# Optimization experiments

Hardware: AMD Instinct MI355X
Metric: run time of the kernel (lower is better)

The kernel has to match this reference:

```python
import jax, jax.numpy as jnp
import numpy as np

EPS = 1e-5  # F.instance_norm default eps


def _patch_attn(x, s):
    """Per-(b,c) instance norm over non-overlapping s x s patches, then sigmoid."""
    b, c, h, w = x.shape
    xr = x.reshape(b, c, h // s, s, w // s, s)
    m = jnp.mean(xr, axis=(3, 5), keepdims=True)
    v = jnp.mean((xr - m) ** 2, axis=(3, 5), keepdims=True)  # biased var, as in training-mode instance_norm
    a = jax.nn.sigmoid((xr - m) * jax.lax.rsqrt(v + EPS))
    return a.reshape(b, c, h, w)


def setup_inputs() -> dict:
    key = jax.random.key(0)
    x = jax.random.normal(key, (16, 64, 256, 256), dtype=jnp.float32)
    return {"x": x}


def reference(x):
    p = (2, 1, 0)
    b, c, h, w = x.shape
    out = x
    for pi in p:  # fixed 3 scales (structural loop, not data loop)
        s = h // (2 ** pi)
        attn = _patch_attn(out, s)
        out = 0.5 * out + 0.5 * (attn * out)
    return out
```

## Files before the change

kernel.cpp:

```cpp
#include <hip/hip_runtime.h>

#define PEPS  1e-5f
#define LOG2E 1.4426950408889634f

__device__ __forceinline__ float fast_rcp(float x) { return __builtin_amdgcn_rcpf(x); }

__device__ __forceinline__ float patch_one(float x, float nrs2, float mrs) {
    const float e = __builtin_amdgcn_exp2f(fmaf(x, nrs2, mrs));
    return x * fmaf(0.5f, fast_rcp(1.0f + e), 0.5f);
}

__device__ __forceinline__ void wave_reduce2(float& a, float& b) {
#pragma unroll
    for (int off = 32; off; off >>= 1) {
        a += __shfl_xor(a, off);
        b += __shfl_xor(b, off);
    }
}

__device__ __forceinline__ void gld_lds16(const float* g, float* l) {
    __builtin_amdgcn_global_load_lds(
        (const __attribute__((address_space(1))) void*)g,
        (__attribute__((address_space(3))) void*)l, 16, 0, 0);
}

__global__ __launch_bounds__(1024) void fused_pyramid_pipe(
    const float* __restrict__ in, float* __restrict__ out)
{
    constexpr int W   = 256;
    constexpr int IMG = W * W;
    __shared__ float tile[32768];
    __shared__ float redS[16], redQ[16];
    __shared__ float redS2[16], redQ2[16];

    const int tid   = threadIdx.x;
    const int wave  = tid >> 6;
    const int lane  = tid & 63;
    const int pr    = wave >> 2;
    const int pc    = wave & 3;
    const int rlane = lane >> 4;
    const int c4    = lane & 15;
    const int bid   = blockIdx.x;

    {
        const float* src = in + (size_t)bid * IMG;
#pragma unroll
        for (int i = 0; i < 8; ++i) {
            const int chunk = wave * 8 + i;
            gld_lds16(src + chunk * 256 + lane * 4, &tile[chunk * 256]);
        }
    }

    for (int k = 0; k < 4; ++k) {
        const int img = bid + k * 256;
        const float* in_img  = in  + (size_t)img * IMG;
        float*       out_img = out + (size_t)img * IMG;

        asm volatile("s_waitcnt vmcnt(0)" ::: "memory");
        __syncthreads();

        float4 v[16];
        float s = 0.f, q = 0.f;
        if (wave < 8) {
            const float* tl = &tile[(pr * 64) * W + pc * 64];
#pragma unroll
            for (int u = 0; u < 16; ++u) {
                const int r = u * 4 + rlane;
                const float4 t = *reinterpret_cast<const float4*>(tl + r * W + c4 * 4);
                v[u] = t;
                s += (t.x + t.y) + (t.z + t.w);
                q = fmaf(t.x, t.x, fmaf(t.y, t.y, fmaf(t.z, t.z, fmaf(t.w, t.w, q))));
            }
        } else {
            const float* gl = in_img + (size_t)(pr * 64) * W + pc * 64;
#pragma unroll
            for (int u = 0; u < 16; ++u) {
                const int r = u * 4 + rlane;
                const float4 t = *reinterpret_cast<const float4*>(gl + (size_t)r * W + c4 * 4);
                v[u] = t;
                s += (t.x + t.y) + (t.z + t.w);
                q = fmaf(t.x, t.x, fmaf(t.y, t.y, fmaf(t.z, t.z, fmaf(t.w, t.w, q))));
            }
        }

        wave_reduce2(s, q);
        float m  = s * (1.0f / 4096.0f);
        float rs = rsqrtf(fmaf(-m, m, q * (1.0f / 4096.0f)) + PEPS);
        float nrs2 = rs * -LOG2E;
        float mrs  = m * rs * LOG2E;

        float s2 = 0.f, q2 = 0.f;
#pragma unroll
        for (int u = 0; u < 16; ++u) {
            float4 t = v[u];
            t.x = patch_one(t.x, nrs2, mrs);
            t.y = patch_one(t.y, nrs2, mrs);
            t.z = patch_one(t.z, nrs2, mrs);
            t.w = patch_one(t.w, nrs2, mrs);
            v[u] = t;
            s2 += (t.x + t.y) + (t.z + t.w);
            q2 = fmaf(t.x, t.x, fmaf(t.y, t.y, fmaf(t.z, t.z, fmaf(t.w, t.w, q2))));
        }

        wave_reduce2(s2, q2);
        if (lane == 0) { redS[wave] = s2; redQ[wave] = q2; }
        __syncthreads();

        if (k < 3) {
            const float* src = in + (size_t)(bid + (k + 1) * 256) * IMG;
#pragma unroll
            for (int i = 0; i < 8; ++i) {
                const int chunk = wave * 8 + i;
                gld_lds16(src + chunk * 256 + lane * 4, &tile[chunk * 256]);
            }
        }

        const int w00 = wave & ~5;
        {
            const float S = (redS[w00] + redS[w00 + 1]) + (redS[w00 + 4] + redS[w00 + 5]);
            const float Q = (redQ[w00] + redQ[w00 + 1]) + (redQ[w00 + 4] + redQ[w00 + 5]);
            m  = S * (1.0f / 16384.0f);
            rs = rsqrtf(fmaf(-m, m, Q * (1.0f / 16384.0f)) + PEPS);
        }
        nrs2 = rs * -LOG2E;
        mrs  = m * rs * LOG2E;

        float s3 = 0.f, q3 = 0.f;
#pragma unroll
        for (int u = 0; u < 16; ++u) {
            float4 t = v[u];
            t.x = patch_one(t.x, nrs2, mrs);
            t.y = patch_one(t.y, nrs2, mrs);
            t.z = patch_one(t.z, nrs2, mrs);
            t.w = patch_one(t.w, nrs2, mrs);
            v[u] = t;
            s3 += (t.x + t.y) + (t.z + t.w);
            q3 = fmaf(t.x, t.x, fmaf(t.y, t.y, fmaf(t.z, t.z, fmaf(t.w, t.w, q3))));
        }

        wave_reduce2(s3, q3);
        if (lane == 0) { redS2[wave] = s3; redQ2[wave] = q3; }
        __syncthreads();
        {
            float S = 0.f, Q = 0.f;
#pragma unroll
            for (int w = 0; w < 16; ++w) { S += redS2[w]; Q += redQ2[w]; }
            m  = S * (1.0f / 65536.0f);
            rs = rsqrtf(fmaf(-m, m, Q * (1.0f / 65536.0f)) + PEPS);
        }
        nrs2 = rs * -LOG2E;
        mrs  = m * rs * LOG2E;

        {
            float* go = out_img + (size_t)(pr * 64) * W + pc * 64;
#pragma unroll
            for (int u = 0; u < 16; ++u) {
                const int r = u * 4 + rlane;
                float4 t = v[u];
                t.x = patch_one(t.x, nrs2, mrs);
                t.y = patch_one(t.y, nrs2, mrs);
                t.z = patch_one(t.z, nrs2, mrs);
                t.w = patch_one(t.w, nrs2, mrs);
                *reinterpret_cast<float4*>(go + (size_t)r * W + c4 * 4) = t;
            }
        }
    }
}

extern "C" void kernel_launch(void* const* d_in, const int* in_sizes, int n_in,
                              void* d_out, int out_size, void* d_ws, size_t ws_size,
                              hipStream_t stream)
{
    const float* x = (const float*)d_in[0];
    float* out = (float*)d_out;
    fused_pyramid_pipe<<<256, 1024, 0, stream>>>(x, out);
}
```

Measured before the change: 113.7 us.

## Balance LDS prefetch and direct loads across all waves with finer waitcnt barriers

Each wave now reads the top half of its 64x64 patch from the LDS prefetch tile and loads the bottom half directly from global memory. Before, waves 0-7 read entirely from LDS and waves 8-15 entirely from global. The LDS tile is remapped to hold the first 32 rows of each patch row-band, and the output row mapping is adjusted to match. __syncthreads is replaced with raw s_barrier, explicit waitcnts and sched_barriers, so global loads for the current image can be issued without draining in-flight prefetches (vmcnt(16)). This evens out load latency across waves and trims barrier overhead. The cost is reliance on exact counter-based waits, which could break if the compiler reorders memory operations.

```diff
diff --git a/kernel.cpp b/kernel.cpp
--- a/kernel.cpp
+++ b/kernel.cpp
@@ -24,7 +24,7 @@
         (__attribute__((address_space(3))) void*)l, 16, 0, 0);
 }
 
-__global__ __launch_bounds__(1024) void fused_pyramid_pipe(
+__global__ __launch_bounds__(1024) void fused_pyramid_pipe2(
     const float* __restrict__ in, float* __restrict__ out)
 {
     constexpr int W   = 256;
@@ -42,45 +42,49 @@
     const int c4    = lane & 15;
     const int bid   = blockIdx.x;
 
-    {
-        const float* src = in + (size_t)bid * IMG;
+    auto prefetch_img = [&](const float* src) {
 #pragma unroll
         for (int i = 0; i < 8; ++i) {
-            const int chunk = wave * 8 + i;
-            gld_lds16(src + chunk * 256 + lane * 4, &tile[chunk * 256]);
+            const int c  = wave * 8 + i;
+            const int gr = ((c >> 5) << 6) + (c & 31);
+            gld_lds16(src + gr * W + lane * 4, &tile[c * W]);
         }
-    }
+    };
+
+    prefetch_img(in + (size_t)bid * IMG);
 
     for (int k = 0; k < 4; ++k) {
         const int img = bid + k * 256;
         const float* in_img  = in  + (size_t)img * IMG;
         float*       out_img = out + (size_t)img * IMG;
 
-        asm volatile("s_waitcnt vmcnt(0)" ::: "memory");
-        __syncthreads();
+        if (k == 0) { asm volatile("s_waitcnt vmcnt(0)" ::: "memory"); }
+        else        { asm volatile("s_waitcnt vmcnt(16)" ::: "memory"); }
+        __builtin_amdgcn_s_barrier();
+        __builtin_amdgcn_sched_barrier(0);
 
         float4 v[16];
+        const float* gl = in_img + (size_t)(pr * 64 + 32) * W + pc * 64;
+#pragma unroll
+        for (int u = 0; u < 8; ++u) {
+            const int r = u * 4 + rlane;
+            v[8 + u] = *reinterpret_cast<const float4*>(gl + (size_t)r * W + c4 * 4);
+        }
+        const float* tl = &tile[(pr * 32) * W + pc * 64];
         float s = 0.f, q = 0.f;
-        if (wave < 8) {
-            const float* tl = &tile[(pr * 64) * W + pc * 64];
 #pragma unroll
-            for (int u = 0; u < 16; ++u) {
-                const int r = u * 4 + rlane;
-                const float4 t = *reinterpret_cast<const float4*>(tl + r * W + c4 * 4);
-                v[u] = t;
-                s += (t.x + t.y) + (t.z + t.w);
-                q = fmaf(t.x, t.x, fmaf(t.y, t.y, fmaf(t.z, t.z, fmaf(t.w, t.w, q))));
-            }
-        } else {
-            const float* gl = in_img + (size_t)(pr * 64) * W + pc * 64;
+        for (int u = 0; u < 8; ++u) {
+            const int r = u * 4 + rlane;
+            const float4 t = *reinterpret_cast<const float4*>(tl + r * W + c4 * 4);
+            v[u] = t;
+            s += (t.x + t.y) + (t.z + t.w);
+            q = fmaf(t.x, t.x, fmaf(t.y, t.y, fmaf(t.z, t.z, fmaf(t.w, t.w, q))));
+        }
 #pragma unroll
-            for (int u = 0; u < 16; ++u) {
-                const int r = u * 4 + rlane;
-                const float4 t = *reinterpret_cast<const float4*>(gl + (size_t)r * W + c4 * 4);
-                v[u] = t;
-                s += (t.x + t.y) + (t.z + t.w);
-                q = fmaf(t.x, t.x, fmaf(t.y, t.y, fmaf(t.z, t.z, fmaf(t.w, t.w, q))));
-            }
+        for (int u = 8; u < 16; ++u) {
+            const float4 t = v[u];
+            s += (t.x + t.y) + (t.z + t.w);
+            q = fmaf(t.x, t.x, fmaf(t.y, t.y, fmaf(t.z, t.z, fmaf(t.w, t.w, q))));
         }
 
         wave_reduce2(s, q);
@@ -104,16 +108,12 @@
 
         wave_reduce2(s2, q2);
         if (lane == 0) { redS[wave] = s2; redQ[wave] = q2; }
-        __syncthreads();
+        asm volatile("s_waitcnt lgkmcnt(0)" ::: "memory");
+        __builtin_amdgcn_s_barrier();
+        __builtin_amdgcn_sched_barrier(0);
 
-        if (k < 3) {
-            const float* src = in + (size_t)(bid + (k + 1) * 256) * IMG;
-#pragma unroll
-            for (int i = 0; i < 8; ++i) {
-                const int chunk = wave * 8 + i;
-                gld_lds16(src + chunk * 256 + lane * 4, &tile[chunk * 256]);
-            }
-        }
+        if (k < 3) prefetch_img(in + (size_t)(bid + (k + 1) * 256) * IMG);
+        __builtin_amdgcn_sched_barrier(0);
 
         const int w00 = wave & ~5;
         {
@@ -140,7 +140,9 @@
 
         wave_reduce2(s3, q3);
         if (lane == 0) { redS2[wave] = s3; redQ2[wave] = q3; }
-        __syncthreads();
+        asm volatile("s_waitcnt lgkmcnt(0)" ::: "memory");
+        __builtin_amdgcn_s_barrier();
+        __builtin_amdgcn_sched_barrier(0);
         {
             float S = 0.f, Q = 0.f;
 #pragma unroll
@@ -155,7 +157,7 @@
             float* go = out_img + (size_t)(pr * 64) * W + pc * 64;
 #pragma unroll
             for (int u = 0; u < 16; ++u) {
-                const int r = u * 4 + rlane;
+                const int r = ((u >> 3) << 5) + ((u & 7) << 2) + rlane;
                 float4 t = v[u];
                 t.x = patch_one(t.x, nrs2, mrs);
                 t.y = patch_one(t.y, nrs2, mrs);
@@ -173,5 +175,5 @@
 {
     const float* x = (const float*)d_in[0];
     float* out = (float*)d_out;
-    fused_pyramid_pipe<<<256, 1024, 0, stream>>>(x, out);
+    fused_pyramid_pipe2<<<256, 1024, 0, stream>>>(x, out);
 }
```

New measurement: 144.8 us. +27.4%, slower.
